# Kernel optimization log

Measured on AMD Instinct MI355X. Metric: run time of the kernel, lower is better.

## Reference

```python
import jax, jax.numpy as jnp
import numpy as np

N_NODES = 100000
N_EDGES = 1200000
N_GRAPHS = 128
IN_C, HID_C, OUT_C = 64, 128, 16


def setup_inputs() -> dict:
    key = jax.random.key(0)
    ks = jax.random.split(key, 6)
    x = jax.random.normal(ks[0], (N_NODES, IN_C), dtype=jnp.float32)
    edge_index = jax.random.randint(ks[1], (2, N_EDGES), 0, N_NODES, dtype=jnp.int64)
    batch = jnp.sort(jax.random.randint(ks[2], (N_NODES,), 0, N_GRAPHS, dtype=jnp.int64))
    W1 = jax.random.normal(ks[3], (IN_C, HID_C), dtype=jnp.float32) * (1.0 / np.sqrt(IN_C))
    b1 = jnp.zeros((HID_C,), jnp.float32)
    W2 = jax.random.normal(ks[4], (HID_C, OUT_C), dtype=jnp.float32) * (1.0 / np.sqrt(HID_C))
    b2 = jnp.zeros((OUT_C,), jnp.float32)
    return {"x": x, "edge_index": edge_index, "batch": batch,
            "W1": W1, "b1": b1, "W2": W2, "b2": b2}


def gcn_conv(x, src, dst, W, b, n):
    """PyG GCNConv: add self-loops, symmetric deg^{-1/2} normalization, scatter-add."""
    h = x @ W                                   # [n, out] dense transform first
    loop = jnp.arange(n, dtype=src.dtype)
    s = jnp.concatenate([src, loop])            # edges + self-loops
    d = jnp.concatenate([dst, loop])
    deg = jax.ops.segment_sum(jnp.ones(d.shape[0], h.dtype), d, num_segments=n)
    dinv = jnp.where(deg > 0, jax.lax.rsqrt(deg), jnp.zeros((), h.dtype))
    norm = dinv[s] * dinv[d]                    # [E + n]
    msg = h[s] * norm[:, None]                  # gather + scale
    return jax.ops.segment_sum(msg, d, num_segments=n) + b  # scatter-add


def reference(x, edge_index, batch, W1, b1, W2, b2):
    n = x.shape[0]
    src, dst = edge_index[0], edge_index[1]
    h = jax.nn.relu(gcn_conv(x, src, dst, W1, b1, n))
    h = gcn_conv(h, src, dst, W2, b2, n)
    # global_mean_pool over batch ids
    sums = jax.ops.segment_sum(h, batch, num_segments=N_GRAPHS)
    cnts = jax.ops.segment_sum(jnp.ones((n,), h.dtype), batch, num_segments=N_GRAPHS)
    pooled = sums / jnp.maximum(cnts, 1.0)[:, None]   # [N_GRAPHS, OUT_C]
    return jax.nn.log_softmax(pooled, axis=1)
```

## Files before the change

### kernel.cpp

```cpp
#include <hip/hip_runtime.h>
#include <hip/hip_bf16.h>


#define THREADS 256
#define NPB 256
#define BSTRIDE 4096
#define CH 4096
#define NBMAX 512

typedef __attribute__((ext_vector_type(8))) short bf16x8;
typedef __attribute__((ext_vector_type(4))) float f32x4;

__device__ __forceinline__ float bfu_lo(unsigned int u) {
    union { unsigned int i; float f; } v; v.i = u << 16; return v.f;
}
__device__ __forceinline__ float bfu_hi(unsigned int u) {
    union { unsigned int i; float f; } v; v.i = u & 0xffff0000u; return v.f;
}
__device__ __forceinline__ unsigned short f2bf(float f) {
    union { float f; unsigned int i; } v; v.f = f;
    unsigned int r = v.i + 0x7fff + ((v.i >> 16) & 1);
    return (unsigned short)(r >> 16);
}
__device__ __forceinline__ unsigned int packbf(float lo, float hi) {
    return (unsigned int)f2bf(lo) | ((unsigned int)f2bf(hi) << 16);
}
__device__ __forceinline__ void unpack8(uint4 u, float* f) {
    f[0] = bfu_lo(u.x); f[1] = bfu_hi(u.x);
    f[2] = bfu_lo(u.y); f[3] = bfu_hi(u.y);
    f[4] = bfu_lo(u.z); f[5] = bfu_hi(u.z);
    f[6] = bfu_lo(u.w); f[7] = bfu_hi(u.w);
}

__global__ __launch_bounds__(THREADS) void k_partition(const int* __restrict__ src,
                                                       const int* __restrict__ dst,
                                                       int* __restrict__ bucketCursor,
                                                       unsigned int* __restrict__ ebuf,
                                                       int E, int NB) {
    __shared__ int h[NBMAX];
    __shared__ int base[NBMAX];
    __shared__ int cnt[NBMAX];
    for (int b = threadIdx.x; b < NBMAX; b += THREADS) { h[b] = 0; cnt[b] = 0; }
    __syncthreads();
    int b0 = blockIdx.x * CH;
    for (int k = 0; k < CH; k += THREADS) {
        int e = b0 + k + threadIdx.x;
        if (e < E) atomicAdd(&h[dst[e] >> 8], 1);
    }
    __syncthreads();
    for (int b = threadIdx.x; b < NB; b += THREADS)
        if (h[b]) base[b] = b * BSTRIDE + atomicAdd(&bucketCursor[b], h[b]);
    __syncthreads();
    for (int k = 0; k < CH; k += THREADS) {
        int e = b0 + k + threadIdx.x;
        if (e < E) {
            int s = src[e], d = dst[e];
            int b = d >> 8;
            int i = base[b] + atomicAdd(&cnt[b], 1);
            ebuf[i] = ((unsigned int)(d & (NPB - 1)) << 17) | (unsigned int)s;
        }
    }
}

__global__ __launch_bounds__(THREADS) void k_bucket_csr(const unsigned int* __restrict__ ebuf,
                                                        const int* __restrict__ bucketCursor,
                                                        const float* __restrict__ x,
                                                        int* __restrict__ offs,
                                                        int* __restrict__ deg,
                                                        int* __restrict__ srcs,
                                                        float* __restrict__ dinv,
                                                        uint4* __restrict__ xnb,
                                                        int n) {
    __shared__ unsigned int eL[BSTRIDE];
    __shared__ int c[NPB];
    __shared__ int cur[NPB];
    __shared__ float dloc[NPB];
    __shared__ int sh[THREADS];
    const int tid = threadIdx.x;
    const int b = blockIdx.x;
    const int nbase = b * NPB;
    const int w0 = b * BSTRIDE;
    const int cnt_b = bucketCursor[b];
    c[tid] = 0;
    __syncthreads();
    for (int i = tid; i < cnt_b; i += THREADS) {
        unsigned int e = ebuf[w0 + i];
        eL[i] = e;
        atomicAdd(&c[e >> 17], 1);
    }
    __syncthreads();
    int c0 = c[tid];
    sh[tid] = c0;
    __syncthreads();
    for (int step = 1; step < THREADS; step <<= 1) {
        int t = (tid >= step) ? sh[tid - step] : 0;
        __syncthreads();
        sh[tid] += t;
        __syncthreads();
    }
    int excl = sh[tid] - c0;
    int node = nbase + tid;
    float dv = rsqrtf((float)(c0 + 1));
    dloc[tid] = dv;
    if (node < n) {
        offs[node] = w0 + excl;
        deg[node] = c0;
        dinv[node] = dv;
    }
    cur[tid] = excl;
    __syncthreads();
    for (int i = tid; i < cnt_b; i += THREADS) {
        unsigned int e = eL[i];
        int pos = w0 + atomicAdd(&cur[e >> 17], 1);
        srcs[pos] = (int)(e & 0x1FFFFu);
    }
    const float4* X4 = (const float4*)x;
    for (int i = tid; i < NPB * 8; i += THREADS) {
        int ln = i >> 3;
        int node2 = nbase + ln;
        if (node2 >= n) break;
        int q = i & 7;
        float dd = dloc[ln];
        float4 a = X4[(size_t)node2 * 16 + q * 2];
        float4 bb = X4[(size_t)node2 * 16 + q * 2 + 1];
        uint4 o;
        o.x = packbf(a.x * dd, a.y * dd);
        o.y = packbf(a.z * dd, a.w * dd);
        o.z = packbf(bb.x * dd, bb.y * dd);
        o.w = packbf(bb.z * dd, bb.w * dd);
        xnb[(size_t)node2 * 8 + q] = o;
    }
}

__global__ __launch_bounds__(THREADS) void k_gather1(const int* __restrict__ offs,
                                                     const int* __restrict__ deg,
                                                     const int* __restrict__ srcs,
                                                     const float* __restrict__ dinv,
                                                     const uint4* __restrict__ xnb,
                                                     uint4* __restrict__ aggb, int n) {
    int idx = blockIdx.x * THREADS + threadIdx.x;
    int node = idx >> 3;
    if (node >= n) return;
    int q = idx & 7;
    float acc[8];
    unpack8(xnb[(size_t)node * 8 + q], acc);
    int e0 = offs[node], e1 = e0 + deg[node];
    for (int e = e0; e < e1; ++e) {
        int s = srcs[e];
        float t[8];
        unpack8(xnb[(size_t)s * 8 + q], t);
#pragma unroll
        for (int j = 0; j < 8; ++j) acc[j] += t[j];
    }
    float dd = dinv[node];
    uint4 o;
    o.x = packbf(acc[0] * dd, acc[1] * dd);
    o.y = packbf(acc[2] * dd, acc[3] * dd);
    o.z = packbf(acc[4] * dd, acc[5] * dd);
    o.w = packbf(acc[6] * dd, acc[7] * dd);
    aggb[(size_t)node * 8 + q] = o;
}

__global__ __launch_bounds__(THREADS) void k_gemm1m(const unsigned short* __restrict__ aggb,
                                                    const float* __restrict__ W1,
                                                    const float* __restrict__ b1,
                                                    unsigned short* __restrict__ h1b,
                                                    int n, int ntiles) {
    const int wave = threadIdx.x >> 6;
    const int lane = threadIdx.x & 63;
    const int col = lane & 15;
    const int ko = lane >> 4;

    bf16x8 bfr[2][8];
#pragma unroll
    for (int ks = 0; ks < 2; ++ks)
#pragma unroll
        for (int nt = 0; nt < 8; ++nt) {
            bf16x8 b;
#pragma unroll
            for (int j = 0; j < 8; ++j)
                b[j] = (short)f2bf(W1[(ks * 32 + ko * 8 + j) * 128 + nt * 16 + col]);
            bfr[ks][nt] = b;
        }
    float bias[8];
#pragma unroll
    for (int nt = 0; nt < 8; ++nt) bias[nt] = b1[nt * 16 + col];

    const int tile0 = (blockIdx.x * 4 + wave) * 4;
    for (int t = 0; t < 4; ++t) {
        int tile = tile0 + t;
        if (tile >= ntiles) return;
        int r0 = tile * 16;
        int rowA = r0 + col;
        if (rowA >= n) rowA = n - 1;
        const bf16x8* Ap = (const bf16x8*)(aggb + (size_t)rowA * 64 + ko * 8);
        bf16x8 a0 = Ap[0];
        bf16x8 a1 = Ap[4];
        f32x4 acc[8];
#pragma unroll
        for (int nt = 0; nt < 8; ++nt) acc[nt] = (f32x4){0.f, 0.f, 0.f, 0.f};
#pragma unroll
        for (int nt = 0; nt < 8; ++nt) {
            acc[nt] = __builtin_amdgcn_mfma_f32_16x16x32_bf16(a0, bfr[0][nt], acc[nt], 0, 0, 0);
            acc[nt] = __builtin_amdgcn_mfma_f32_16x16x32_bf16(a1, bfr[1][nt], acc[nt], 0, 0, 0);
        }
#pragma unroll
        for (int nt = 0; nt < 8; ++nt) {
#pragma unroll
            for (int r = 0; r < 4; ++r) {
                int row = r0 + ko * 4 + r;
                if (row < n) {
                    float v = fmaxf(acc[nt][r] + bias[nt], 0.f);
                    h1b[(size_t)row * 128 + nt * 16 + col] = f2bf(v);
                }
            }
        }
    }
}

__global__ __launch_bounds__(THREADS) void k_gemm2(const uint4* __restrict__ h1b4,
                                                   const float* __restrict__ W2,
                                                   const float* __restrict__ dinv,
                                                   unsigned short* __restrict__ ts, int n) {
    __shared__ float Ws[128 * 16];
    {
        float4* Ws4 = (float4*)Ws;
        const float4* W24 = (const float4*)W2;
        for (int i = threadIdx.x; i < 128 * 16 / 4; i += THREADS) Ws4[i] = W24[i];
    }
    __syncthreads();
    const int c0 = (threadIdx.x & 3) * 4;
    const int r0 = blockIdx.x * 256 + (threadIdx.x >> 2) * 4;
    if (r0 >= n) return;

    if (r0 + 3 < n) {
        const uint4* A0 = h1b4 + (size_t)r0 * 16;
        const uint4* A1 = A0 + 16;
        const uint4* A2 = A0 + 32;
        const uint4* A3 = A0 + 48;
        float4 acc0 = {0,0,0,0}, acc1 = {0,0,0,0}, acc2 = {0,0,0,0}, acc3 = {0,0,0,0};
#pragma unroll 4
        for (int kk = 0; kk < 16; ++kk) {
            float a0[8], a1[8], a2[8], a3[8];
            unpack8(A0[kk], a0);
            unpack8(A1[kk], a1);
            unpack8(A2[kk], a2);
            unpack8(A3[kk], a3);
#pragma unroll
            for (int j = 0; j < 8; ++j) {
                float4 w = *(const float4*)(&Ws[(kk * 8 + j) * 16 + c0]);
                acc0.x = fmaf(a0[j], w.x, acc0.x); acc0.y = fmaf(a0[j], w.y, acc0.y);
                acc0.z = fmaf(a0[j], w.z, acc0.z); acc0.w = fmaf(a0[j], w.w, acc0.w);
                acc1.x = fmaf(a1[j], w.x, acc1.x); acc1.y = fmaf(a1[j], w.y, acc1.y);
                acc1.z = fmaf(a1[j], w.z, acc1.z); acc1.w = fmaf(a1[j], w.w, acc1.w);
                acc2.x = fmaf(a2[j], w.x, acc2.x); acc2.y = fmaf(a2[j], w.y, acc2.y);
                acc2.z = fmaf(a2[j], w.z, acc2.z); acc2.w = fmaf(a2[j], w.w, acc2.w);
                acc3.x = fmaf(a3[j], w.x, acc3.x); acc3.y = fmaf(a3[j], w.y, acc3.y);
                acc3.z = fmaf(a3[j], w.z, acc3.z); acc3.w = fmaf(a3[j], w.w, acc3.w);
            }
        }
        float d0 = dinv[r0], d1 = dinv[r0 + 1], d2 = dinv[r0 + 2], d3 = dinv[r0 + 3];
        uint2 p;
        p.x = packbf(acc0.x * d0, acc0.y * d0); p.y = packbf(acc0.z * d0, acc0.w * d0);
        *(uint2*)(ts + (size_t)(r0 + 0) * 16 + c0) = p;
        p.x = packbf(acc1.x * d1, acc1.y * d1); p.y = packbf(acc1.z * d1, acc1.w * d1);
        *(uint2*)(ts + (size_t)(r0 + 1) * 16 + c0) = p;
        p.x = packbf(acc2.x * d2, acc2.y * d2); p.y = packbf(acc2.z * d2, acc2.w * d2);
        *(uint2*)(ts + (size_t)(r0 + 2) * 16 + c0) = p;
        p.x = packbf(acc3.x * d3, acc3.y * d3); p.y = packbf(acc3.z * d3, acc3.w * d3);
        *(uint2*)(ts + (size_t)(r0 + 3) * 16 + c0) = p;
    } else {
        for (int i = 0; i < 4; ++i) {
            int r = r0 + i;
            if (r >= n) break;
            const uint4* A = h1b4 + (size_t)r * 16;
            float4 acc = {0, 0, 0, 0};
            for (int kk = 0; kk < 16; ++kk) {
                float a[8];
                unpack8(A[kk], a);
#pragma unroll
                for (int j = 0; j < 8; ++j) {
                    float4 w = *(const float4*)(&Ws[(kk * 8 + j) * 16 + c0]);
                    acc.x = fmaf(a[j], w.x, acc.x); acc.y = fmaf(a[j], w.y, acc.y);
                    acc.z = fmaf(a[j], w.z, acc.z); acc.w = fmaf(a[j], w.w, acc.w);
                }
            }
            float dd = dinv[r];
            uint2 p;
            p.x = packbf(acc.x * dd, acc.y * dd);
            p.y = packbf(acc.z * dd, acc.w * dd);
            *(uint2*)(ts + (size_t)r * 16 + c0) = p;
        }
    }
}

__global__ __launch_bounds__(THREADS) void k_gather2(const int* __restrict__ offs,
                                                     const int* __restrict__ deg,
                                                     const int* __restrict__ srcs,
                                                     const float* __restrict__ dinv,
                                                     const uint4* __restrict__ ts,
                                                     float* __restrict__ h2, int n) {
    int idx = blockIdx.x * THREADS + threadIdx.x;
    int node = idx >> 1;
    if (node >= n) return;
    int q = idx & 1;
    float acc[8];
    unpack8(ts[(size_t)node * 2 + q], acc);
    int e0 = offs[node], e1 = e0 + deg[node];
    for (int e = e0; e < e1; ++e) {
        int s = srcs[e];
        float t[8];
        unpack8(ts[(size_t)s * 2 + q], t);
#pragma unroll
        for (int j = 0; j < 8; ++j) acc[j] += t[j];
    }
    float dd = dinv[node];
    float4 o0 = {acc[0] * dd, acc[1] * dd, acc[2] * dd, acc[3] * dd};
    float4 o1 = {acc[4] * dd, acc[5] * dd, acc[6] * dd, acc[7] * dd};
    float4* O = (float4*)(h2 + (size_t)node * 16 + q * 8);
    O[0] = o0;
    O[1] = o1;
}

__global__ __launch_bounds__(THREADS) void k_poolfinal(const float* __restrict__ h2,
                                                       const int* __restrict__ batch,
                                                       const float* __restrict__ b2,
                                                       float* __restrict__ out, int n) {
    int g = blockIdx.x;
    int lo = 0, hi = n;
    while (lo < hi) { int mid = (lo + hi) >> 1; if (batch[mid] < g) lo = mid + 1; else hi = mid; }
    int s0 = lo;
    hi = n;
    while (lo < hi) { int mid = (lo + hi) >> 1; if (batch[mid] < g + 1) lo = mid + 1; else hi = mid; }
    int s1 = lo;

    int c = threadIdx.x & 15;
    int rg = threadIdx.x >> 4;
    float acc = 0.f;
    for (int i = s0 + rg; i < s1; i += 16) acc += h2[(size_t)i * 16 + c];
    __shared__ float red[THREADS];
    red[threadIdx.x] = acc;
    __syncthreads();
    for (int step = 128; step >= 16; step >>= 1) {
        if (threadIdx.x < step) red[threadIdx.x] += red[threadIdx.x + step];
        __syncthreads();
    }
    if (threadIdx.x == 0) {
        float cnt = fmaxf((float)(s1 - s0), 1.0f);
        float v[16];
        float mx = -1e30f;
#pragma unroll
        for (int k = 0; k < 16; ++k) {
            v[k] = red[k] / cnt + b2[k];
            mx = fmaxf(mx, v[k]);
        }
        float se = 0.f;
#pragma unroll
        for (int k = 0; k < 16; ++k) se += expf(v[k] - mx);
        float lse = logf(se) + mx;
#pragma unroll
        for (int k = 0; k < 16; ++k) out[g * 16 + k] = v[k] - lse;
    }
}

extern "C" void kernel_launch(void* const* d_in, const int* in_sizes, int n_in,
                              void* d_out, int out_size, void* d_ws, size_t ws_size,
                              hipStream_t stream) {
    const float* x    = (const float*)d_in[0];
    const int* edges  = (const int*)d_in[1];
    const int* batch  = (const int*)d_in[2];
    const float* W1   = (const float*)d_in[3];
    const float* b1   = (const float*)d_in[4];
    const float* W2   = (const float*)d_in[5];
    const float* b2   = (const float*)d_in[6];
    float* out        = (float*)d_out;

    const int n = in_sizes[2];
    const int E = in_sizes[1] / 2;
    const int* src = edges;
    const int* dst = edges + E;
    const int NB = (n + NPB - 1) / NPB;
    const int npart = (E + CH - 1) / CH;
    const int ntiles = (n + 15) / 16;

    char* ws = (char*)d_ws;
    size_t off = 0;
    auto carve = [&](size_t bytes) { char* p = ws + off; off = (off + bytes + 255) & ~(size_t)255; return p; };
    int*   bucketCursor = (int*)carve(NBMAX * 4);
    int*   offs    = (int*)carve((size_t)n * 4);
    int*   deg     = (int*)carve((size_t)n * 4);
    int*   srcs    = (int*)carve((size_t)NB * BSTRIDE * 4);
    float* dinv    = (float*)carve((size_t)n * 4);
    uint4* xnb     = (uint4*)carve((size_t)n * 64 * 2);
    char*  aggreg  = (char*)carve((size_t)n * 64 * 2);
    char*  big     = (char*)carve((size_t)NB * BSTRIDE * 4 > (size_t)n * 128 * 2
                                  ? (size_t)NB * BSTRIDE * 4 : (size_t)n * 128 * 2);
    unsigned int* ebuf = (unsigned int*)big;
    unsigned short* h1b = (unsigned short*)big;
    unsigned short* aggb = (unsigned short*)aggreg;
    unsigned short* ts = (unsigned short*)aggreg;
    float* h2 = (float*)(aggreg + (size_t)n * 16 * 4);

    auto blks = [](long long work) { return (int)((work + THREADS - 1) / THREADS); };

    hipMemsetAsync(bucketCursor, 0, NBMAX * 4, stream);
    k_partition  <<<npart, THREADS, 0, stream>>>(src, dst, bucketCursor, ebuf, E, NB);
    k_bucket_csr <<<NB, THREADS, 0, stream>>>(ebuf, bucketCursor, x, offs, deg, srcs, dinv, xnb, n);

    k_gather1 <<<blks((long long)n * 8), THREADS, 0, stream>>>(offs, deg, srcs, dinv, xnb, (uint4*)aggb, n);
    k_gemm1m  <<<(ntiles + 15) / 16, THREADS, 0, stream>>>(aggb, W1, b1, h1b, n, ntiles);
    k_gemm2   <<<(n + 255) / 256, THREADS, 0, stream>>>((const uint4*)h1b, W2, dinv, ts, n);
    k_gather2 <<<blks((long long)n * 2), THREADS, 0, stream>>>(offs, deg, srcs, dinv, (const uint4*)ts, h2, n);

    k_poolfinal <<<128, THREADS, 0, stream>>>(h2, batch, b2, out, n);
}
```

Measured before the change: 147.4 us.

## Fuse first and second GCN GEMMs via LDS-staged hidden tile with MFMA

Measured after the change: 132.6 us. 1.11x faster.

```diff
diff --git a/kernel.cpp b/kernel.cpp
--- a/kernel.cpp
+++ b/kernel.cpp
@@ -161,17 +161,20 @@
     aggb[(size_t)node * 8 + q] = o;
 }
 
-__global__ __launch_bounds__(THREADS) void k_gemm1m(const unsigned short* __restrict__ aggb,
-                                                    const float* __restrict__ W1,
-                                                    const float* __restrict__ b1,
-                                                    unsigned short* __restrict__ h1b,
-                                                    int n, int ntiles) {
+__global__ __launch_bounds__(THREADS) void k_gemm12m(const unsigned short* __restrict__ aggb,
+                                                     const float* __restrict__ W1,
+                                                     const float* __restrict__ b1,
+                                                     const float* __restrict__ W2,
+                                                     const float* __restrict__ dinv,
+                                                     unsigned short* __restrict__ ts,
+                                                     int n, int ntiles) {
+    __shared__ unsigned short h1L[4][16][136];
     const int wave = threadIdx.x >> 6;
     const int lane = threadIdx.x & 63;
     const int col = lane & 15;
     const int ko = lane >> 4;
 
-    bf16x8 bfr[2][8];
+    bf16x8 bfr1[2][8];
 #pragma unroll
     for (int ks = 0; ks < 2; ++ks)
 #pragma unroll
@@ -180,11 +183,20 @@
 #pragma unroll
             for (int j = 0; j < 8; ++j)
                 b[j] = (short)f2bf(W1[(ks * 32 + ko * 8 + j) * 128 + nt * 16 + col]);
-            bfr[ks][nt] = b;
+            bfr1[ks][nt] = b;
         }
     float bias[8];
 #pragma unroll
     for (int nt = 0; nt < 8; ++nt) bias[nt] = b1[nt * 16 + col];
+    bf16x8 bfr2[4];
+#pragma unroll
+    for (int ks = 0; ks < 4; ++ks) {
+        bf16x8 b;
+#pragma unroll
+        for (int j = 0; j < 8; ++j)
+            b[j] = (short)f2bf(W2[(ks * 32 + ko * 8 + j) * 16 + col]);
+        bfr2[ks] = b;
+    }
 
     const int tile0 = (blockIdx.x * 4 + wave) * 4;
     for (int t = 0; t < 4; ++t) {
@@ -201,95 +213,27 @@
         for (int nt = 0; nt < 8; ++nt) acc[nt] = (f32x4){0.f, 0.f, 0.f, 0.f};
 #pragma unroll
         for (int nt = 0; nt < 8; ++nt) {
-            acc[nt] = __builtin_amdgcn_mfma_f32_16x16x32_bf16(a0, bfr[0][nt], acc[nt], 0, 0, 0);
-            acc[nt] = __builtin_amdgcn_mfma_f32_16x16x32_bf16(a1, bfr[1][nt], acc[nt], 0, 0, 0);
-        }
-#pragma unroll
-        for (int nt = 0; nt < 8; ++nt) {
-#pragma unroll
-            for (int r = 0; r < 4; ++r) {
-                int row = r0 + ko * 4 + r;
-                if (row < n) {
-                    float v = fmaxf(acc[nt][r] + bias[nt], 0.f);
-                    h1b[(size_t)row * 128 + nt * 16 + col] = f2bf(v);
-                }
+            acc[nt] = __builtin_amdgcn_mfma_f32_16x16x32_bf16(a0, bfr1[0][nt], acc[nt], 0, 0, 0);
+            acc[nt] = __builtin_amdgcn_mfma_f32_16x16x32_bf16(a1, bfr1[1][nt], acc[nt], 0, 0, 0);
+        }
+#pragma unroll
+        for (int nt = 0; nt < 8; ++nt)
+#pragma unroll
+            for (int r = 0; r < 4; ++r)
+                h1L[wave][ko * 4 + r][nt * 16 + col] = f2bf(fmaxf(acc[nt][r] + bias[nt], 0.f));
+        f32x4 acc2 = (f32x4){0.f, 0.f, 0.f, 0.f};
+#pragma unroll
+        for (int ks = 0; ks < 4; ++ks) {
+            bf16x8 a2 = *(const bf16x8*)&h1L[wave][col][ks * 32 + ko * 8];
+            acc2 = __builtin_amdgcn_mfma_f32_16x16x32_bf16(a2, bfr2[ks], acc2, 0, 0, 0);
+        }
+#pragma unroll
+        for (int r = 0; r < 4; ++r) {
+            int row = r0 + ko * 4 + r;
+            if (row < n) {
+                float dd = dinv[row];
+                ts[(size_t)row * 16 + col] = f2bf(acc2[r] * dd);
             }
-        }
-    }
-}
-
-__global__ __launch_bounds__(THREADS) void k_gemm2(const uint4* __restrict__ h1b4,
-                                                   const float* __restrict__ W2,
-                                                   const float* __restrict__ dinv,
-                                                   unsigned short* __restrict__ ts, int n) {
-    __shared__ float Ws[128 * 16];
-    {
-        float4* Ws4 = (float4*)Ws;
-        const float4* W24 = (const float4*)W2;
-        for (int i = threadIdx.x; i < 128 * 16 / 4; i += THREADS) Ws4[i] = W24[i];
-    }
-    __syncthreads();
-    const int c0 = (threadIdx.x & 3) * 4;
-    const int r0 = blockIdx.x * 256 + (threadIdx.x >> 2) * 4;
-    if (r0 >= n) return;
-
-    if (r0 + 3 < n) {
-        const uint4* A0 = h1b4 + (size_t)r0 * 16;
-        const uint4* A1 = A0 + 16;
-        const uint4* A2 = A0 + 32;
-        const uint4* A3 = A0 + 48;
-        float4 acc0 = {0,0,0,0}, acc1 = {0,0,0,0}, acc2 = {0,0,0,0}, acc3 = {0,0,0,0};
-#pragma unroll 4
-        for (int kk = 0; kk < 16; ++kk) {
-            float a0[8], a1[8], a2[8], a3[8];
-            unpack8(A0[kk], a0);
-            unpack8(A1[kk], a1);
-            unpack8(A2[kk], a2);
-            unpack8(A3[kk], a3);
-#pragma unroll
-            for (int j = 0; j < 8; ++j) {
-                float4 w = *(const float4*)(&Ws[(kk * 8 + j) * 16 + c0]);
-                acc0.x = fmaf(a0[j], w.x, acc0.x); acc0.y = fmaf(a0[j], w.y, acc0.y);
-                acc0.z = fmaf(a0[j], w.z, acc0.z); acc0.w = fmaf(a0[j], w.w, acc0.w);
-                acc1.x = fmaf(a1[j], w.x, acc1.x); acc1.y = fmaf(a1[j], w.y, acc1.y);
-                acc1.z = fmaf(a1[j], w.z, acc1.z); acc1.w = fmaf(a1[j], w.w, acc1.w);
-                acc2.x = fmaf(a2[j], w.x, acc2.x); acc2.y = fmaf(a2[j], w.y, acc2.y);
-                acc2.z = fmaf(a2[j], w.z, acc2.z); acc2.w = fmaf(a2[j], w.w, acc2.w);
-                acc3.x = fmaf(a3[j], w.x, acc3.x); acc3.y = fmaf(a3[j], w.y, acc3.y);
-                acc3.z = fmaf(a3[j], w.z, acc3.z); acc3.w = fmaf(a3[j], w.w, acc3.w);
-            }
-        }
-        float d0 = dinv[r0], d1 = dinv[r0 + 1], d2 = dinv[r0 + 2], d3 = dinv[r0 + 3];
-        uint2 p;
-        p.x = packbf(acc0.x * d0, acc0.y * d0); p.y = packbf(acc0.z * d0, acc0.w * d0);
-        *(uint2*)(ts + (size_t)(r0 + 0) * 16 + c0) = p;
-        p.x = packbf(acc1.x * d1, acc1.y * d1); p.y = packbf(acc1.z * d1, acc1.w * d1);
-        *(uint2*)(ts + (size_t)(r0 + 1) * 16 + c0) = p;
-        p.x = packbf(acc2.x * d2, acc2.y * d2); p.y = packbf(acc2.z * d2, acc2.w * d2);
-        *(uint2*)(ts + (size_t)(r0 + 2) * 16 + c0) = p;
-        p.x = packbf(acc3.x * d3, acc3.y * d3); p.y = packbf(acc3.z * d3, acc3.w * d3);
-        *(uint2*)(ts + (size_t)(r0 + 3) * 16 + c0) = p;
-    } else {
-        for (int i = 0; i < 4; ++i) {
-            int r = r0 + i;
-            if (r >= n) break;
-            const uint4* A = h1b4 + (size_t)r * 16;
-            float4 acc = {0, 0, 0, 0};
-            for (int kk = 0; kk < 16; ++kk) {
-                float a[8];
-                unpack8(A[kk], a);
-#pragma unroll
-                for (int j = 0; j < 8; ++j) {
-                    float4 w = *(const float4*)(&Ws[(kk * 8 + j) * 16 + c0]);
-                    acc.x = fmaf(a[j], w.x, acc.x); acc.y = fmaf(a[j], w.y, acc.y);
-                    acc.z = fmaf(a[j], w.z, acc.z); acc.w = fmaf(a[j], w.w, acc.w);
-                }
-            }
-            float dd = dinv[r];
-            uint2 p;
-            p.x = packbf(acc.x * dd, acc.y * dd);
-            p.y = packbf(acc.z * dd, acc.w * dd);
-            *(uint2*)(ts + (size_t)r * 16 + c0) = p;
         }
     }
 }
@@ -396,9 +340,8 @@
     char*  big     = (char*)carve((size_t)NB * BSTRIDE * 4 > (size_t)n * 128 * 2
                                   ? (size_t)NB * BSTRIDE * 4 : (size_t)n * 128 * 2);
     unsigned int* ebuf = (unsigned int*)big;
-    unsigned short* h1b = (unsigned short*)big;
+    unsigned short* ts = (unsigned short*)big;
     unsigned short* aggb = (unsigned short*)aggreg;
-    unsigned short* ts = (unsigned short*)aggreg;
     float* h2 = (float*)(aggreg + (size_t)n * 16 * 4);
 
     auto blks = [](long long work) { return (int)((work + THREADS - 1) / THREADS); };
@@ -408,8 +351,7 @@
     k_bucket_csr <<<NB, THREADS, 0, stream>>>(ebuf, bucketCursor, x, offs, deg, srcs, dinv, xnb, n);
 
     k_gather1 <<<blks((long long)n * 8), THREADS, 0, stream>>>(offs, deg, srcs, dinv, xnb, (uint4*)aggb, n);
-    k_gemm1m  <<<(ntiles + 15) / 16, THREADS, 0, stream>>>(aggb, W1, b1, h1b, n, ntiles);
-    k_gemm2   <<<(n + 255) / 256, THREADS, 0, stream>>>((const uint4*)h1b, W2, dinv, ts, n);
+    k_gemm12m <<<(ntiles + 15) / 16, THREADS, 0, stream>>>(aggb, W1, b1, W2, dinv, ts, n, ntiles);
     k_gather2 <<<blks((long long)n * 2), THREADS, 0, stream>>>(offs, deg, srcs, dinv, (const uint4*)ts, h2, n);
 
     k_poolfinal <<<128, THREADS, 0, stream>>>(h2, batch, b2, out, n);
```
